# Performance work log

Hardware: AMD Instinct MI355X
Metric: run time of the kernel (lower is better)

The kernel has to match this reference:

```python
import jax, jax.numpy as jnp
import numpy as np
import math

B, N, E, H = 2, 2048, 1024, 16
D = E // H

def setup_inputs() -> dict:
    key = jax.random.key(0)
    ks = jax.random.split(key, 5)
    scale = 1.0 / math.sqrt(E)  # approx xavier_uniform std
    x = jax.random.normal(ks[0], (B, N, E), dtype=jnp.float32)
    Wq = jax.random.normal(ks[1], (E, E), dtype=jnp.float32) * scale
    Wk = jax.random.normal(ks[2], (E, E), dtype=jnp.float32) * scale
    Wv = jax.random.normal(ks[3], (E, E), dtype=jnp.float32) * scale
    Wo = jax.random.normal(ks[4], (E, E), dtype=jnp.float32) * scale
    zeros = jnp.zeros((E,), dtype=jnp.float32)
    rho_logit = jnp.full((1,), math.log(0.95 / 0.05), dtype=jnp.float32)
    return {"x": x, "Wq": Wq, "bq": zeros, "Wk": Wk, "bk": zeros,
            "Wv": Wv, "bv": zeros, "Wo": Wo, "bo": zeros,
            "rho_logit": rho_logit}

def reference(x, Wq, bq, Wk, bk, Wv, bv, Wo, bo, rho_logit):
    # QKV projections (torch Linear: y = x @ W.T + b)
    q = (x @ Wq.T + bq).reshape(B, N, H, D).transpose(0, 2, 1, 3)  # [B,H,N,D]
    k = (x @ Wk.T + bk).reshape(B, N, H, D).transpose(0, 2, 1, 3)
    v = (x @ Wv.T + bv).reshape(B, N, H, D).transpose(0, 2, 1, 3)
    # rho is read via .item() in the torch forward -> treated as a constant
    rho = jax.lax.stop_gradient(jax.nn.sigmoid(rho_logit[0]))
    # pure InfSA: rho^{|i-j|} distance-decayed scores, no softmax
    idx = jnp.arange(N)
    dist = jnp.abs(idx[:, None] - idx[None, :]).astype(jnp.float32)  # [N,N]
    decay = rho ** dist
    scores = jnp.einsum('bhnd,bhsd->bhns', q, k) / math.sqrt(D) * decay  # [B,H,N,N]
    out = jnp.einsum('bhns,bhsd->bhnd', scores, v)  # [B,H,N,D]
    out = out.transpose(0, 2, 1, 3).reshape(B, N, E)
    return out @ Wo.T + bo
```

## Files before the change

### kernel.cpp

```cpp
#include <hip/hip_runtime.h>
#include <hip/hip_bf16.h>
#include <stdint.h>

constexpr int Bc  = 2;
constexpr int Nn_ = 2048;
constexpr int Ee  = 1024;
constexpr int Hh  = 16;
constexpr int Dd  = 64;
constexpr int Mm  = Bc * Nn_;

constexpr int QB = 128;
constexpr int KB = 64;
constexpr int WB = 256;

typedef __bf16  bf16x8  __attribute__((ext_vector_type(8)));
typedef float   f32x4   __attribute__((ext_vector_type(4)));
typedef unsigned short ushort8 __attribute__((ext_vector_type(8)));

__device__ inline unsigned short f2bf(float f) {
    union { __hip_bfloat16 h; unsigned short u; } cv;
    cv.h = __float2bfloat16(f);
    return cv.u;
}
__device__ inline uint32_t pk2bf(float a, float b) {
    return (uint32_t)f2bf(a) | ((uint32_t)f2bf(b) << 16);
}

__device__ inline void gload_lds16(const void* g, void* l) {
    __builtin_amdgcn_global_load_lds((__attribute__((address_space(1))) void*)g,
                                     (__attribute__((address_space(3))) void*)l,
                                     16, 0, 0);
}

__global__ __launch_bounds__(256)
void conv_all(const float* __restrict__ x,  const float* __restrict__ Wq,
              const float* __restrict__ Wk, const float* __restrict__ Wv,
              const float* __restrict__ Wo,
              unsigned short* __restrict__ xbf, unsigned short* __restrict__ wqkv,
              unsigned short* __restrict__ wobf)
{
    const int b = blockIdx.x;
    const float* in;
    unsigned short* out;
    int off;
    if (b < 2048)      { in = x;  out = xbf;                 off = b * 2048; }
    else if (b < 2560) { in = Wq; out = wqkv;                off = (b - 2048) * 2048; }
    else if (b < 3072) { in = Wk; out = wqkv + (1 << 20);    off = (b - 2560) * 2048; }
    else if (b < 3584) { in = Wv; out = wqkv + (2 << 20);    off = (b - 3072) * 2048; }
    else               { in = Wo; out = wobf;                off = (b - 3584) * 2048; }
    const int i = off + threadIdx.x * 8;
    float4 a = *(const float4*)(in + i);
    float4 c = *(const float4*)(in + i + 4);
    ushort8 o;
    o[0] = f2bf(a.x); o[1] = f2bf(a.y); o[2] = f2bf(a.z); o[3] = f2bf(a.w);
    o[4] = f2bf(c.x); o[5] = f2bf(c.y); o[6] = f2bf(c.z); o[7] = f2bf(c.w);
    *(ushort8*)(out + i) = o;
}

__global__ __launch_bounds__(512, 2)
void gemm_qkv(const unsigned short* __restrict__ A, const unsigned short* __restrict__ Bw,
              const float* __restrict__ b0, const float* __restrict__ b1,
              const float* __restrict__ b2,
              unsigned short* __restrict__ C0, unsigned short* __restrict__ C1,
              unsigned short* __restrict__ C2)
{
    constexpr int K  = 1024;
    constexpr int NT = K / 64;

    __shared__ unsigned short As[2][256 * 64];
    __shared__ unsigned short Bs[2][256 * 64];

    const int bid = blockIdx.x;
    const int swz = (bid & 7) * 24 + (bid >> 3);
    const int m0  = (swz / 12) * 256;
    const int n0  = (swz % 12) * 256;

    const int t  = threadIdx.x;
    const int w  = t >> 6;
    const int l  = t & 63;
    const int lr = l & 15;
    const int lg = l >> 4;
    const int wr = w >> 2;
    const int wc = w & 3;
    const int r8 = l >> 3;
    const int ch = (l & 7) ^ r8;
    const int x7 = l & 7;

    f32x4 acc[8][4];
#pragma unroll
    for (int i = 0; i < 8; ++i)
#pragma unroll
        for (int j = 0; j < 4; ++j)
            acc[i][j] = (f32x4){0.f, 0.f, 0.f, 0.f};

    const unsigned short* Ag = A  + (size_t)(m0 + w * 32 + r8) * K + ch * 8;
    const unsigned short* Bg = Bw + (size_t)(n0 + w * 32 + r8) * K + ch * 8;

    auto STAGE = [&](int buf, int k0) {
#pragma unroll
        for (int c = 0; c < 4; ++c)
            gload_lds16(Ag + (size_t)(c * 8) * K + k0, &As[buf][(w * 32 + c * 8) * 64]);
#pragma unroll
        for (int c = 0; c < 4; ++c)
            gload_lds16(Bg + (size_t)(c * 8) * K + k0, &Bs[buf][(w * 32 + c * 8) * 64]);
    };

    STAGE(0, 0);
    STAGE(1, 64);
    asm volatile("s_waitcnt vmcnt(8)" ::: "memory");
    __builtin_amdgcn_s_barrier();

    int cur = 0;
    for (int kt = 0; kt < NT; ++kt) {
        bf16x8 a[8][2], b[4][2];
#pragma unroll
        for (int i = 0; i < 8; ++i) {
            const int row = wr * 128 + i * 16 + lr;
#pragma unroll
            for (int kk = 0; kk < 2; ++kk)
                a[i][kk] = *(const bf16x8*)&As[cur][row * 64 + (((kk * 4 + lg) ^ x7) * 8)];
        }
#pragma unroll
        for (int j = 0; j < 4; ++j) {
            const int row = wc * 64 + j * 16 + lr;
#pragma unroll
            for (int kk = 0; kk < 2; ++kk)
                b[j][kk] = *(const bf16x8*)&Bs[cur][row * 64 + (((kk * 4 + lg) ^ x7) * 8)];
        }
        asm volatile("s_waitcnt lgkmcnt(0)" ::: "memory");
        __builtin_amdgcn_sched_barrier(0);
        __builtin_amdgcn_s_barrier();

        if (kt + 2 < NT) {
            STAGE(cur, (kt + 2) * 64);
            asm volatile("s_waitcnt vmcnt(8)" ::: "memory");
        } else {
            asm volatile("s_waitcnt vmcnt(0)" ::: "memory");
        }

        __builtin_amdgcn_s_setprio(1);
#pragma unroll
        for (int kk = 0; kk < 2; ++kk)
#pragma unroll
            for (int i = 0; i < 8; ++i)
#pragma unroll
                for (int j = 0; j < 4; ++j)
                    acc[i][j] = __builtin_amdgcn_mfma_f32_16x16x32_bf16(a[i][kk], b[j][kk], acc[i][j], 0, 0, 0);
        __builtin_amdgcn_s_setprio(0);

        __builtin_amdgcn_s_barrier();
        cur ^= 1;
    }

    const int proj = n0 >> 10;
#pragma unroll
    for (int i = 0; i < 8; ++i) {
#pragma unroll
        for (int j = 0; j < 4; ++j) {
            const int mb  = m0 + wr * 128 + i * 16 + lg * 4;
            const int n_g = n0 + wc * 64 + j * 16 + lr;
            const int nn  = n_g & 1023;
            const int h   = nn >> 6, d = nn & 63;
            const int bb  = mb >> 11, nq = mb & 2047;
            const float bs = (proj == 0 ? b0 : proj == 1 ? b1 : b2)[nn];
            if (proj == 2) {
                uint2 p;
                p.x = pk2bf(acc[i][j][0] + bs, acc[i][j][1] + bs);
                p.y = pk2bf(acc[i][j][2] + bs, acc[i][j][3] + bs);
                *(uint2*)&C2[(((size_t)bb * Hh + h) * Dd + d) * Nn_ + nq] = p;
            } else {
                unsigned short* Cb = (proj == 0 ? C0 : C1);
                const float sc = (proj == 0) ? 0.125f : 1.0f;
                unsigned short* base = &Cb[(((size_t)bb * Hh + h) * Nn_ + nq) * Dd + d];
#pragma unroll
                for (int r = 0; r < 4; ++r)
                    base[r * Dd] = f2bf((acc[i][j][r] + bs) * sc);
            }
        }
    }
}

template<int BM, int BN>
__global__ __launch_bounds__(256)
void gemm_o(const unsigned short* __restrict__ A, const unsigned short* __restrict__ Bw,
            const float* __restrict__ b0, float* __restrict__ C0,
            int Nc, int K, int ntx)
{
    constexpr int WM = BM / 2, WN = BN / 2;
    constexpr int FI = WM / 16, FJ = WN / 16;
    constexpr int AI = BM / 32;
    constexpr int BI = BN / 32;

    __shared__ unsigned short As[BM * 64];
    __shared__ unsigned short Bs[BN * 64];

    const int nwg = gridDim.x;
    const int bid = blockIdx.x;
    const int swz = (bid & 7) * (nwg >> 3) + (bid >> 3);
    const int m0  = (swz / ntx) * BM;
    const int n0  = (swz % ntx) * BN;

    const int t  = threadIdx.x;
    const int w  = t >> 6;
    const int l  = t & 63;
    const int lr = l & 15;
    const int lg = l >> 4;
    const int wr = w >> 1, wc = w & 1;

    f32x4 acc[FI][FJ];
#pragma unroll
    for (int i = 0; i < FI; ++i)
#pragma unroll
        for (int j = 0; j < FJ; ++j)
            acc[i][j] = (f32x4){0.f, 0.f, 0.f, 0.f};

    const int r8 = l >> 3;
    const int ch = (l & 7) ^ r8;
    const unsigned short* Ag = A  + (size_t)(m0 + w * (BM / 4) + r8) * K + ch * 8;
    const unsigned short* Bg = Bw + (size_t)(n0 + w * (BN / 4) + r8) * K + ch * 8;
    const int x7a = (l & 7);

    for (int k0 = 0; k0 < K; k0 += 64) {
        __syncthreads();
#pragma unroll
        for (int c = 0; c < AI; ++c)
            gload_lds16(Ag + (size_t)(c * 8) * K + k0, As + (w * (BM / 4) + c * 8) * 64);
#pragma unroll
        for (int c = 0; c < BI; ++c)
            gload_lds16(Bg + (size_t)(c * 8) * K + k0, Bs + (w * (BN / 4) + c * 8) * 64);
        __syncthreads();

        bf16x8 a[FI][2], b[FJ][2];
#pragma unroll
        for (int i = 0; i < FI; ++i) {
            const int row = wr * WM + i * 16 + lr;
#pragma unroll
            for (int kk = 0; kk < 2; ++kk)
                a[i][kk] = *(const bf16x8*)&As[row * 64 + (((kk * 4 + lg) ^ x7a) * 8)];
        }
#pragma unroll
        for (int j = 0; j < FJ; ++j) {
            const int row = wc * WN + j * 16 + lr;
#pragma unroll
            for (int kk = 0; kk < 2; ++kk)
                b[j][kk] = *(const bf16x8*)&Bs[row * 64 + (((kk * 4 + lg) ^ x7a) * 8)];
        }
#pragma unroll
        for (int kk = 0; kk < 2; ++kk)
#pragma unroll
            for (int i = 0; i < FI; ++i)
#pragma unroll
                for (int j = 0; j < FJ; ++j)
                    acc[i][j] = __builtin_amdgcn_mfma_f32_16x16x32_bf16(a[i][kk], b[j][kk], acc[i][j], 0, 0, 0);
    }

#pragma unroll
    for (int i = 0; i < FI; ++i) {
#pragma unroll
        for (int j = 0; j < FJ; ++j) {
            const int mb  = m0 + wr * WM + i * 16 + lg * 4;
            const int n_g = n0 + wc * WN + j * 16 + lr;
            const float bs = b0[n_g];
#pragma unroll
            for (int r = 0; r < 4; ++r)
                C0[(size_t)(mb + r) * Nc + n_g] = acc[i][j][r] + bs;
        }
    }
}

__global__ __launch_bounds__(256)
void attn_mfma(const unsigned short* __restrict__ qg, const unsigned short* __restrict__ kg,
               const unsigned short* __restrict__ vtg, unsigned short* __restrict__ outg,
               const float* __restrict__ rho_logit)
{
    __shared__ unsigned short Kl[2][64 * 64];
    __shared__ unsigned short Vl[2][64 * 64];
    __shared__ unsigned short Pl[4][32 * 64];

    const int t  = threadIdx.x;
    const int w  = t >> 6;
    const int l  = t & 63;
    const int lr = l & 15;
    const int lg = l >> 4;
    const int l7 = l & 7;
    const int l8 = l >> 3;

    const int bh = blockIdx.y;
    const int i0 = blockIdx.x * QB;

    const unsigned short* qp = qg  + ((size_t)bh * Nn_ + i0 + w * 32) * Dd;
    const unsigned short* kp = kg  + (size_t)bh * Nn_ * Dd;
    const unsigned short* vp = vtg + (size_t)bh * Dd * Nn_;

    const float rho = 1.0f / (1.0f + expf(-rho_logit[0]));
    const float l2r = log2f(rho);

    bf16x8 qf[2][2];
#pragma unroll
    for (int jq = 0; jq < 2; ++jq)
#pragma unroll
        for (int st = 0; st < 2; ++st)
            qf[jq][st] = *(const bf16x8*)(qp + (jq * 16 + lr) * Dd + st * 32 + lg * 8);

    float eq[2], eqi[2];
#pragma unroll
    for (int jq = 0; jq < 2; ++jq) {
        const float d = (float)(w * 32 + jq * 16 + lr);
        eq[jq]  = exp2f(d * l2r);
        eqi[jq] = exp2f(-d * l2r);
    }
    float es[4], esi[4];
#pragma unroll
    for (int r = 0; r < 4; ++r) {
        const float d = (float)(lg * 4 + r);
        es[r]  = exp2f(-d * l2r);
        esi[r] = exp2f(d * l2r);
    }
    float p16[4], p16i[4];
#pragma unroll
    for (int js = 0; js < 4; ++js) {
        p16[js]  = exp2f(16.f * js * l2r);
        p16i[js] = exp2f(-16.f * js * l2r);
    }

    f32x4 acc_o[4][2];
#pragma unroll
    for (int jd = 0; jd < 4; ++jd)
#pragma unroll
        for (int jq = 0; jq < 2; ++jq)
            acc_o[jd][jq] = (f32x4){0.f, 0.f, 0.f, 0.f};

    const int lo = (i0 - WB) > 0 ? (i0 - WB) : 0;
    const int hi = (i0 + QB + WB) < Nn_ ? (i0 + QB + WB) : Nn_;
    const int chnk = (l7 ^ l8) * 8;

    auto STAGEKV = [&](int buf, int s0) {
        gload_lds16(kp + (size_t)(s0 + (2 * w + 0) * 8 + l8) * Dd + chnk, &Kl[buf][(2 * w + 0) * 512]);
        gload_lds16(kp + (size_t)(s0 + (2 * w + 1) * 8 + l8) * Dd + chnk, &Kl[buf][(2 * w + 1) * 512]);
        gload_lds16(vp + (size_t)((2 * w + 0) * 8 + l8) * Nn_ + s0 + chnk, &Vl[buf][(2 * w + 0) * 512]);
        gload_lds16(vp + (size_t)((2 * w + 1) * 8 + l8) * Nn_ + s0 + chnk, &Vl[buf][(2 * w + 1) * 512]);
    };

    STAGEKV(0, lo);
    __syncthreads();
    int cur = 0;

    for (int s0 = lo; s0 < hi; s0 += KB) {
        if (s0 + KB < hi) STAGEKV(cur ^ 1, s0 + KB);

        f32x4 sa[4][2];
#pragma unroll
        for (int js = 0; js < 4; ++js)
#pragma unroll
            for (int jq = 0; jq < 2; ++jq)
                sa[js][jq] = (f32x4){0.f, 0.f, 0.f, 0.f};

        __builtin_amdgcn_s_setprio(1);
#pragma unroll
        for (int st = 0; st < 2; ++st)
#pragma unroll
            for (int js = 0; js < 4; ++js) {
                bf16x8 ak = *(const bf16x8*)&Kl[cur][(js * 16 + lr) * 64 + ((st * 32 + lg * 8) ^ (l7 << 3))];
                sa[js][0] = __builtin_amdgcn_mfma_f32_16x16x32_bf16(ak, qf[0][st], sa[js][0], 0, 0, 0);
                sa[js][1] = __builtin_amdgcn_mfma_f32_16x16x32_bf16(ak, qf[1][st], sa[js][1], 0, 0, 0);
            }
        __builtin_amdgcn_s_setprio(0);

        const float gd  = (float)(i0 - s0);
        const float sb  = exp2f(gd * l2r);
        const float sbi = exp2f(-gd * l2r);
#pragma unroll
        for (int js = 0; js < 4; ++js)
#pragma unroll
            for (int jq = 0; jq < 2; ++jq) {
                const float c1 = sb * eq[jq] * p16i[js];
                const float c2 = sbi * eqi[jq] * p16[js];
                float pv0 = sa[js][jq][0] * fminf(c1 * es[0], c2 * esi[0]);
                float pv1 = sa[js][jq][1] * fminf(c1 * es[1], c2 * esi[1]);
                float pv2 = sa[js][jq][2] * fminf(c1 * es[2], c2 * esi[2]);
                float pv3 = sa[js][jq][3] * fminf(c1 * es[3], c2 * esi[3]);
                uint2 pk;
                pk.x = pk2bf(pv0, pv1);
                pk.y = pk2bf(pv2, pv3);
                *(uint2*)&Pl[w][(jq * 16 + lr) * 64 + ((js * 16 + lg * 4) ^ (l7 << 3))] = pk;
            }

        __builtin_amdgcn_s_setprio(1);
#pragma unroll
        for (int st = 0; st < 2; ++st) {
            bf16x8 pb0 = *(const bf16x8*)&Pl[w][(0 * 16 + lr) * 64 + ((st * 32 + lg * 8) ^ (l7 << 3))];
            bf16x8 pb1 = *(const bf16x8*)&Pl[w][(1 * 16 + lr) * 64 + ((st * 32 + lg * 8) ^ (l7 << 3))];
#pragma unroll
            for (int jd = 0; jd < 4; ++jd) {
                bf16x8 av = *(const bf16x8*)&Vl[cur][(jd * 16 + lr) * 64 + ((st * 32 + lg * 8) ^ (l7 << 3))];
                acc_o[jd][0] = __builtin_amdgcn_mfma_f32_16x16x32_bf16(av, pb0, acc_o[jd][0], 0, 0, 0);
                acc_o[jd][1] = __builtin_amdgcn_mfma_f32_16x16x32_bf16(av, pb1, acc_o[jd][1], 0, 0, 0);
            }
        }
        __builtin_amdgcn_s_setprio(0);

        __syncthreads();
        cur ^= 1;
    }

    const int bb = bh >> 4, h = bh & 15;
#pragma unroll
    for (int jd = 0; jd < 4; ++jd)
#pragma unroll
        for (int jq = 0; jq < 2; ++jq) {
            uint2 pk;
            pk.x = pk2bf(acc_o[jd][jq][0], acc_o[jd][jq][1]);
            pk.y = pk2bf(acc_o[jd][jq][2], acc_o[jd][jq][3]);
            *(uint2*)&outg[((size_t)bb * Nn_ + i0 + w * 32 + jq * 16 + lr) * Ee
                           + h * 64 + jd * 16 + lg * 4] = pk;
        }
}

extern "C" void kernel_launch(void* const* d_in, const int* in_sizes, int n_in,
                              void* d_out, int out_size, void* d_ws, size_t ws_size,
                              hipStream_t stream)
{
    const float* x         = (const float*)d_in[0];
    const float* Wq        = (const float*)d_in[1];
    const float* bq        = (const float*)d_in[2];
    const float* Wk        = (const float*)d_in[3];
    const float* bk        = (const float*)d_in[4];
    const float* Wv        = (const float*)d_in[5];
    const float* bv        = (const float*)d_in[6];
    const float* Wo        = (const float*)d_in[7];
    const float* bo        = (const float*)d_in[8];
    const float* rho_logit = (const float*)d_in[9];
    float* outp = (float*)d_out;

    const size_t sz  = (size_t)Mm * Ee;
    const size_t wsz = (size_t)Ee * Ee;

    unsigned short* xbf  = (unsigned short*)d_ws;
    unsigned short* wqkv = xbf + sz;
    unsigned short* wobf = wqkv + 3 * wsz;
    unsigned short* qb   = wobf + wsz;
    unsigned short* kb   = qb + sz;
    unsigned short* vtb  = kb + sz;
    unsigned short* abf  = vtb + sz;

    conv_all<<<dim3(4096), dim3(256), 0, stream>>>(x, Wq, Wk, Wv, Wo, xbf, wqkv, wobf);

    gemm_qkv<<<dim3(192), dim3(512), 0, stream>>>(xbf, wqkv, bq, bk, bv, qb, kb, vtb);

    dim3 gatt(Nn_ / QB, Bc * Hh);
    attn_mfma<<<gatt, dim3(256), 0, stream>>>(qb, kb, vtb, abf, rho_logit);

    gemm_o<128, 64><<<dim3(512), dim3(256), 0, stream>>>(abf, wobf, bo, outp, Ee, Ee, 16);
}
```

Baseline: 93.72 us.

## Shrink QKV GEMM tiles to 128x128, drop double buffering, transpose MFMA for Q/K stores

The QKV projection GEMM now uses 128x128 tiles with 256 threads and 768 blocks instead of 256x256 tiles with 512 threads and 192 blocks. It uses a single LDS buffer with __syncthreads in place of the double-buffered, hand-scheduled pipeline. For the Q and K outputs the MFMA operands are swapped so each lane holds 4 consecutive d values, which allows packed 8-byte stores with a vectorized bias load instead of scalar 2-byte stores. The aim is better CU occupancy and coalesced epilogue writes, at the cost of losing load/compute overlap and getting less operand reuse per tile.

```diff
diff --git a/kernel.cpp b/kernel.cpp
--- a/kernel.cpp
+++ b/kernel.cpp
@@ -57,38 +57,37 @@
     *(ushort8*)(out + i) = o;
 }
 
-__global__ __launch_bounds__(512, 2)
+__global__ __launch_bounds__(256)
 void gemm_qkv(const unsigned short* __restrict__ A, const unsigned short* __restrict__ Bw,
               const float* __restrict__ b0, const float* __restrict__ b1,
               const float* __restrict__ b2,
               unsigned short* __restrict__ C0, unsigned short* __restrict__ C1,
               unsigned short* __restrict__ C2)
 {
-    constexpr int K  = 1024;
-    constexpr int NT = K / 64;
-
-    __shared__ unsigned short As[2][256 * 64];
-    __shared__ unsigned short Bs[2][256 * 64];
+    constexpr int K = 1024;
+
+    __shared__ unsigned short As[128 * 64];
+    __shared__ unsigned short Bs[128 * 64];
 
     const int bid = blockIdx.x;
-    const int swz = (bid & 7) * 24 + (bid >> 3);
-    const int m0  = (swz / 12) * 256;
-    const int n0  = (swz % 12) * 256;
+    const int swz = (bid & 7) * 96 + (bid >> 3);
+    const int m0  = (swz / 24) * 128;
+    const int n0  = (swz % 24) * 128;
+    const int proj = n0 >> 10;
 
     const int t  = threadIdx.x;
     const int w  = t >> 6;
     const int l  = t & 63;
     const int lr = l & 15;
     const int lg = l >> 4;
-    const int wr = w >> 2;
-    const int wc = w & 3;
+    const int wr = w >> 1, wc = w & 1;
     const int r8 = l >> 3;
     const int ch = (l & 7) ^ r8;
     const int x7 = l & 7;
 
-    f32x4 acc[8][4];
-#pragma unroll
-    for (int i = 0; i < 8; ++i)
+    f32x4 acc[4][4];
+#pragma unroll
+    for (int i = 0; i < 4; ++i)
 #pragma unroll
         for (int j = 0; j < 4; ++j)
             acc[i][j] = (f32x4){0.f, 0.f, 0.f, 0.f};
@@ -96,85 +95,84 @@
     const unsigned short* Ag = A  + (size_t)(m0 + w * 32 + r8) * K + ch * 8;
     const unsigned short* Bg = Bw + (size_t)(n0 + w * 32 + r8) * K + ch * 8;
 
-    auto STAGE = [&](int buf, int k0) {
+    for (int k0 = 0; k0 < K; k0 += 64) {
+        __syncthreads();
 #pragma unroll
         for (int c = 0; c < 4; ++c)
-            gload_lds16(Ag + (size_t)(c * 8) * K + k0, &As[buf][(w * 32 + c * 8) * 64]);
+            gload_lds16(Ag + (size_t)(c * 8) * K + k0, &As[(w * 32 + c * 8) * 64]);
 #pragma unroll
         for (int c = 0; c < 4; ++c)
-            gload_lds16(Bg + (size_t)(c * 8) * K + k0, &Bs[buf][(w * 32 + c * 8) * 64]);
-    };
-
-    STAGE(0, 0);
-    STAGE(1, 64);
-    asm volatile("s_waitcnt vmcnt(8)" ::: "memory");
-    __builtin_amdgcn_s_barrier();
-
-    int cur = 0;
-    for (int kt = 0; kt < NT; ++kt) {
-        bf16x8 a[8][2], b[4][2];
-#pragma unroll
-        for (int i = 0; i < 8; ++i) {
-            const int row = wr * 128 + i * 16 + lr;
-#pragma unroll
-            for (int kk = 0; kk < 2; ++kk)
-                a[i][kk] = *(const bf16x8*)&As[cur][row * 64 + (((kk * 4 + lg) ^ x7) * 8)];
+            gload_lds16(Bg + (size_t)(c * 8) * K + k0, &Bs[(w * 32 + c * 8) * 64]);
+        __syncthreads();
+
+        bf16x8 a[4][2], b[4][2];
+#pragma unroll
+        for (int i = 0; i < 4; ++i) {
+            const int row = wr * 64 + i * 16 + lr;
+#pragma unroll
+            for (int kk = 0; kk < 2; ++kk)
+                a[i][kk] = *(const bf16x8*)&As[row * 64 + (((kk * 4 + lg) ^ x7) * 8)];
         }
 #pragma unroll
         for (int j = 0; j < 4; ++j) {
             const int row = wc * 64 + j * 16 + lr;
 #pragma unroll
             for (int kk = 0; kk < 2; ++kk)
-                b[j][kk] = *(const bf16x8*)&Bs[cur][row * 64 + (((kk * 4 + lg) ^ x7) * 8)];
-        }
-        asm volatile("s_waitcnt lgkmcnt(0)" ::: "memory");
-        __builtin_amdgcn_sched_barrier(0);
-        __builtin_amdgcn_s_barrier();
-
-        if (kt + 2 < NT) {
-            STAGE(cur, (kt + 2) * 64);
-            asm volatile("s_waitcnt vmcnt(8)" ::: "memory");
+                b[j][kk] = *(const bf16x8*)&Bs[row * 64 + (((kk * 4 + lg) ^ x7) * 8)];
+        }
+        if (proj == 2) {
+#pragma unroll
+            for (int kk = 0; kk < 2; ++kk)
+#pragma unroll
+                for (int i = 0; i < 4; ++i)
+#pragma unroll
+                    for (int j = 0; j < 4; ++j)
+                        acc[i][j] = __builtin_amdgcn_mfma_f32_16x16x32_bf16(a[i][kk], b[j][kk], acc[i][j], 0, 0, 0);
         } else {
-            asm volatile("s_waitcnt vmcnt(0)" ::: "memory");
-        }
-
-        __builtin_amdgcn_s_setprio(1);
-#pragma unroll
-        for (int kk = 0; kk < 2; ++kk)
-#pragma unroll
-            for (int i = 0; i < 8; ++i)
-#pragma unroll
-                for (int j = 0; j < 4; ++j)
-                    acc[i][j] = __builtin_amdgcn_mfma_f32_16x16x32_bf16(a[i][kk], b[j][kk], acc[i][j], 0, 0, 0);
-        __builtin_amdgcn_s_setprio(0);
-
-        __builtin_amdgcn_s_barrier();
-        cur ^= 1;
-    }
-
-    const int proj = n0 >> 10;
-#pragma unroll
-    for (int i = 0; i < 8; ++i) {
-#pragma unroll
-        for (int j = 0; j < 4; ++j) {
-            const int mb  = m0 + wr * 128 + i * 16 + lg * 4;
-            const int n_g = n0 + wc * 64 + j * 16 + lr;
-            const int nn  = n_g & 1023;
-            const int h   = nn >> 6, d = nn & 63;
-            const int bb  = mb >> 11, nq = mb & 2047;
-            const float bs = (proj == 0 ? b0 : proj == 1 ? b1 : b2)[nn];
-            if (proj == 2) {
+#pragma unroll
+            for (int kk = 0; kk < 2; ++kk)
+#pragma unroll
+                for (int i = 0; i < 4; ++i)
+#pragma unroll
+                    for (int j = 0; j < 4; ++j)
+                        acc[i][j] = __builtin_amdgcn_mfma_f32_16x16x32_bf16(b[j][kk], a[i][kk], acc[i][j], 0, 0, 0);
+        }
+    }
+
+    if (proj == 2) {
+#pragma unroll
+        for (int i = 0; i < 4; ++i) {
+#pragma unroll
+            for (int j = 0; j < 4; ++j) {
+                const int mb  = m0 + wr * 64 + i * 16 + lg * 4;
+                const int n_g = n0 + wc * 64 + j * 16 + lr;
+                const int nn  = n_g & 1023;
+                const int h   = nn >> 6, d = nn & 63;
+                const int bb  = mb >> 11, nq = mb & 2047;
+                const float bs = b2[nn];
                 uint2 p;
                 p.x = pk2bf(acc[i][j][0] + bs, acc[i][j][1] + bs);
                 p.y = pk2bf(acc[i][j][2] + bs, acc[i][j][3] + bs);
                 *(uint2*)&C2[(((size_t)bb * Hh + h) * Dd + d) * Nn_ + nq] = p;
-            } else {
-                unsigned short* Cb = (proj == 0 ? C0 : C1);
-                const float sc = (proj == 0) ? 0.125f : 1.0f;
-                unsigned short* base = &Cb[(((size_t)bb * Hh + h) * Nn_ + nq) * Dd + d];
-#pragma unroll
-                for (int r = 0; r < 4; ++r)
-                    base[r * Dd] = f2bf((acc[i][j][r] + bs) * sc);
+            }
+        }
+    } else {
+        const float* bN = proj ? b1 : b0;
+        unsigned short* CN = proj ? C1 : C0;
+        const float sc = proj ? 1.0f : 0.125f;
+#pragma unroll
+        for (int i = 0; i < 4; ++i) {
+#pragma unroll
+            for (int j = 0; j < 4; ++j) {
+                const int mq = m0 + wr * 64 + i * 16 + lr;
+                const int nn = (n0 & 1023) + wc * 64 + j * 16 + lg * 4;
+                const int h  = nn >> 6, d = nn & 63;
+                const int bb = mq >> 11, nq = mq & 2047;
+                const float4 bv = *(const float4*)&bN[nn];
+                uint2 p;
+                p.x = pk2bf((acc[i][j][0] + bv.x) * sc, (acc[i][j][1] + bv.y) * sc);
+                p.y = pk2bf((acc[i][j][2] + bv.z) * sc, (acc[i][j][3] + bv.w) * sc);
+                *(uint2*)&CN[(((size_t)bb * Hh + h) * Nn_ + nq) * Dd + d] = p;
             }
         }
     }
@@ -445,7 +443,7 @@
 
     conv_all<<<dim3(4096), dim3(256), 0, stream>>>(x, Wq, Wk, Wv, Wo, xbf, wqkv, wobf);
 
-    gemm_qkv<<<dim3(192), dim3(512), 0, stream>>>(xbf, wqkv, bq, bk, bv, qb, kb, vtb);
+    gemm_qkv<<<dim3(768), dim3(256), 0, stream>>>(xbf, wqkv, bq, bk, bv, qb, kb, vtb);
 
     dim3 gatt(Nn_ / QB, Bc * Hh);
     attn_mfma<<<gatt, dim3(256), 0, stream>>>(qb, kb, vtb, abf, rho_logit);
```

Result: slower. 100.9 us (+7.7%).
